# Kernel tuning notes

Hardware: AMD Instinct MI355X
Metric: run time of the kernel (lower is better)

## Reference

```python
import jax, jax.numpy as jnp
import numpy as np

N_NODES, N_EDGES = 100000, 800000
F_NODE, F_EDGE, N_CLASSES = 128, 16, 10


def _lin(key, fan_in, fan_out, bias=True):
    k1, k2 = jax.random.split(key)
    W = jax.random.normal(k1, (fan_in, fan_out), jnp.float32) * 0.05
    if bias:
        b = jax.random.normal(k2, (fan_out,), jnp.float32) * 0.05
        return W, b
    return (W,)


def setup_inputs() -> dict:
    key = jax.random.key(0)
    ks = jax.random.split(key, 24)
    inp = {
        "x": jax.random.normal(ks[0], (N_NODES, F_NODE), jnp.float32),
        "edge_index": jax.random.randint(ks[1], (2, N_EDGES), 0, N_NODES, jnp.int64 if jax.config.jax_enable_x64 else jnp.int32),
        "edge_attr": jax.random.normal(ks[2], (N_EDGES, F_EDGE), jnp.float32),
    }
    dims = [(F_NODE, 128), (128, 128), (128, 256)]  # (in_channels, out_channels) per layer
    i = 3
    for li, (din, dout) in enumerate(dims, start=1):
        inp[f"Wq{li}"], inp[f"bq{li}"] = _lin(ks[i], din, dout); i += 1
        inp[f"Wk{li}"], inp[f"bk{li}"] = _lin(ks[i], din, dout); i += 1
        inp[f"Wv{li}"], inp[f"bv{li}"] = _lin(ks[i], din, dout); i += 1
        (inp[f"We{li}"],) = _lin(ks[i], F_EDGE, dout, bias=False); i += 1  # PyG lin_edge: bias=False
        inp[f"Ws{li}"], inp[f"bs{li}"] = _lin(ks[i], din, dout); i += 1  # root/skip weight
    inp["Wc"], inp["bc"] = _lin(ks[i], 256, N_CLASSES)
    return inp


def transformer_conv(x, src, dst, edge_attr, Wq, bq, Wk, bk, Wv, bv, We, Ws, bs):
    """PyG TransformerConv, heads=1, concat=True, root_weight=True."""
    N = x.shape[0]
    C = Wq.shape[1]
    q = x @ Wq + bq                      # [N, C]
    k = x @ Wk + bk                      # [N, C]
    v = x @ Wv + bv                      # [N, C]
    e = edge_attr @ We                   # [E, C] edge-conditioned term
    # per-edge attention logits: <q_i, k_j + e_ij> / sqrt(C)
    alpha = jnp.sum(q[dst] * (k[src] + e), axis=-1) / jnp.sqrt(jnp.float32(C))  # [E]
    # segment softmax over edges sharing a destination node
    m = jax.ops.segment_max(alpha, dst, num_segments=N)
    p = jnp.exp(alpha - m[dst])
    s = jax.ops.segment_sum(p, dst, num_segments=N)
    a = p / (s[dst] + 1e-16)
    # scatter-aggregate weighted messages (value_j + edge term)
    out = jax.ops.segment_sum(a[:, None] * (v[src] + e), dst, num_segments=N)  # [N, C]
    return out + x @ Ws + bs             # root/skip connection


def reference(x, edge_index, edge_attr,
              Wq1, bq1, Wk1, bk1, Wv1, bv1, We1, Ws1, bs1,
              Wq2, bq2, Wk2, bk2, Wv2, bv2, We2, Ws2, bs2,
              Wq3, bq3, Wk3, bk3, Wv3, bv3, We3, Ws3, bs3,
              Wc, bc):
    src, dst = edge_index[0], edge_index[1]
    h = transformer_conv(x, src, dst, edge_attr, Wq1, bq1, Wk1, bk1, Wv1, bv1, We1, Ws1, bs1)
    h = jax.nn.relu(h)  # dropout is identity in eval mode
    h = transformer_conv(h, src, dst, edge_attr, Wq2, bq2, Wk2, bk2, Wv2, bv2, We2, Ws2, bs2)
    h = jax.nn.relu(h)
    h = transformer_conv(h, src, dst, edge_attr, Wq3, bq3, Wk3, bk3, Wv3, bv3, We3, Ws3, bs3)
    return h @ Wc + bc                   # [N, num_classes]
```

## Files before the change

kernel.cpp:

```cpp
#include <hip/hip_runtime.h>
#include <math.h>


typedef unsigned int uint;
typedef unsigned short ushort;
typedef __bf16 bf16x8 __attribute__((ext_vector_type(8)));
typedef float f32x4 __attribute__((ext_vector_type(4)));

__device__ __forceinline__ ushort f2bf(float f) {
    uint u = __float_as_uint(f);
    u += 0x7fffu + ((u >> 16) & 1u);
    return (ushort)(u >> 16);
}
__device__ __forceinline__ float bf2f(ushort h) {
    return __uint_as_float(((uint)h) << 16);
}
__device__ __forceinline__ void unpack8(uint4 t, float* o) {
    o[0] = bf2f((ushort)(t.x & 0xffffu)); o[1] = bf2f((ushort)(t.x >> 16));
    o[2] = bf2f((ushort)(t.y & 0xffffu)); o[3] = bf2f((ushort)(t.y >> 16));
    o[4] = bf2f((ushort)(t.z & 0xffffu)); o[5] = bf2f((ushort)(t.z >> 16));
    o[6] = bf2f((ushort)(t.w & 0xffffu)); o[7] = bf2f((ushort)(t.w >> 16));
}

__global__ void k_zero(uint* p, int n) {
    int i = blockIdx.x * 256 + threadIdx.x;
    if (i < n) p[i] = 0u;
}

__global__ void k_hist(const int* __restrict__ dst, uint* __restrict__ counts, int E, int N) {
    int e = blockIdx.x * 256 + threadIdx.x;
    if (e < E) {
        int d = dst[e];
        d = (d < 0) ? 0 : (d >= N ? N - 1 : d);
        atomicAdd(&counts[d], 1u);
    }
}

__global__ void k_scan1(const uint* __restrict__ counts, uint* __restrict__ bsum, int n) {
    __shared__ uint sm[256];
    int tid = threadIdx.x;
    int base = blockIdx.x * 1024 + tid * 4;
    uint s = 0;
#pragma unroll
    for (int j = 0; j < 4; ++j)
        if (base + j < n) s += counts[base + j];
    sm[tid] = s;
    __syncthreads();
    for (int d = 128; d > 0; d >>= 1) {
        if (tid < d) sm[tid] += sm[tid + d];
        __syncthreads();
    }
    if (tid == 0) bsum[blockIdx.x] = sm[0];
}

__global__ void k_scan2(uint* bsum, int nb) {
    if (threadIdx.x == 0 && blockIdx.x == 0) {
        uint run = 0;
        for (int i = 0; i < nb; ++i) { uint v = bsum[i]; bsum[i] = run; run += v; }
    }
}

__global__ void k_scan3(const uint* __restrict__ counts, const uint* __restrict__ bsum,
                        uint* __restrict__ row_ptr, int n, int E) {
    __shared__ uint sm[256];
    int tid = threadIdx.x;
    int base = blockIdx.x * 1024 + tid * 4;
    uint local[4];
    uint s = 0;
#pragma unroll
    for (int j = 0; j < 4; ++j) {
        local[j] = (base + j < n) ? counts[base + j] : 0u;
        s += local[j];
    }
    sm[tid] = s;
    __syncthreads();
    for (int d = 1; d < 256; d <<= 1) {
        uint v = (tid >= d) ? sm[tid - d] : 0u;
        __syncthreads();
        sm[tid] += v;
        __syncthreads();
    }
    uint run = sm[tid] - s + bsum[blockIdx.x];
#pragma unroll
    for (int j = 0; j < 4; ++j)
        if (base + j < n) { row_ptr[base + j] = run; run += local[j]; }
    if (blockIdx.x == 0 && tid == 0) row_ptr[n] = (uint)E;
}

__global__ void k_fill(const int* __restrict__ ei, const uint* __restrict__ row_ptr,
                       uint* __restrict__ cursor, int2* __restrict__ srcid, int E, int N) {
    int e = blockIdx.x * 256 + threadIdx.x;
    if (e >= E) return;
    int s = ei[e];
    int d = ei[E + e];
    s = (s < 0) ? 0 : (s >= N ? N - 1 : s);
    d = (d < 0) ? 0 : (d >= N ? N - 1 : d);
    uint idx = row_ptr[d] + atomicAdd(&cursor[d], 1u);
    srcid[idx] = make_int2(s, e);
}

__global__ void k_cvt(const float4* __restrict__ in, ushort4* __restrict__ outp, int n4) {
    int i = blockIdx.x * 256 + threadIdx.x;
    if (i >= n4) return;
    float4 v = in[i];
    ushort4 o;
    o.x = f2bf(v.x); o.y = f2bf(v.y); o.z = f2bf(v.z); o.w = f2bf(v.w);
    outp[i] = o;
}

__global__ void k_packg(const float* __restrict__ Wq, const float* __restrict__ bq,
                        const float* __restrict__ We, float* __restrict__ Wgf,
                        float* __restrict__ bgf, int C) {
    int id = blockIdx.x * 256 + threadIdx.x;
    if (id < 2048) {
        int k = id >> 4, f = id & 15;
        float s = 0.f;
        for (int c = 0; c < C; ++c) s = fmaf(Wq[k * C + c], We[f * C + c], s);
        Wgf[id] = s;
    } else if (id < 2064) {
        int f = id - 2048;
        float s = 0.f;
        for (int c = 0; c < C; ++c) s = fmaf(bq[c], We[f * C + c], s);
        bgf[f] = s;
    }
}

__global__ void k_packw(const float* __restrict__ Wq, const float* __restrict__ Wk,
                        const float* __restrict__ Wv, const float* __restrict__ Ws,
                        const float* __restrict__ Wgf, ushort* __restrict__ Bp, int C) {
    int nct = (4 * C + 16) >> 4;
    int total = 4 * nct * 512;
    int id = blockIdx.x * 256 + threadIdx.x;
    if (id >= total) return;
    int j = id & 7;
    int rest = id >> 3;
    int lane = rest & 63;
    rest >>= 6;
    int ct = rest % nct;
    int kt = rest / nct;
    int k = kt * 32 + ((lane >> 4) << 3) + j;
    int c = (ct << 4) + (lane & 15);
    float w;
    if (c < 4 * C) {
        int mat = c / C, cc = c % C;
        const float* W = (mat == 0) ? Wq : (mat == 1) ? Wk : (mat == 2) ? Wv : Ws;
        w = W[k * C + cc];
    } else {
        w = Wgf[k * 16 + (c - 4 * C)];
    }
    Bp[id] = f2bf(w);
}

__global__ void k_bias(const float* __restrict__ bq, const float* __restrict__ bk,
                       const float* __restrict__ bv, const float* __restrict__ bs,
                       const float* __restrict__ bgf, float* __restrict__ outp, int C) {
    int c = blockIdx.x * 256 + threadIdx.x;
    if (c >= 4 * C + 16) return;
    float v;
    if (c < 4 * C) {
        int mat = c / C, cc = c % C;
        const float* b = (mat == 0) ? bq : (mat == 1) ? bk : (mat == 2) ? bv : bs;
        v = b[cc];
    } else {
        v = bgf[c - 4 * C];
    }
    outp[c] = v;
}

__global__ __launch_bounds__(256) void k_gemm(const ushort* __restrict__ A,
                                              const ushort* __restrict__ Bp,
                                              const float* __restrict__ bias,
                                              ushort* __restrict__ H,
                                              ushort* __restrict__ S,
                                              ushort* __restrict__ g, int C) {
    int fourC = 4 * C, threeC = 3 * C;
    int P = fourC + 16;
    int nct = P >> 4;
    int lane = threadIdx.x & 63;
    int wave = threadIdx.x >> 6;
    int quad = lane >> 4;
    int r = lane & 15;
    int m0 = blockIdx.y << 4;
    int c0 = (blockIdx.x << 8) + (wave << 6);
    int ct0 = c0 >> 4;
    if (ct0 >= nct) return;
    int row = m0 + r;

    f32x4 acc[4];
#pragma unroll
    for (int i = 0; i < 4; ++i) acc[i] = (f32x4){0.f, 0.f, 0.f, 0.f};

#pragma unroll
    for (int kk = 0; kk < 4; ++kk) {
        bf16x8 a = *(const bf16x8*)(A + (size_t)row * 128 + kk * 32 + (quad << 3));
#pragma unroll
        for (int i = 0; i < 4; ++i) {
            if (ct0 + i < nct) {
                bf16x8 b = *(const bf16x8*)(Bp + ((size_t)((kk * nct + ct0 + i) << 6) + lane) * 8);
                acc[i] = __builtin_amdgcn_mfma_f32_16x16x32_bf16(a, b, acc[i], 0, 0, 0);
            }
        }
    }
#pragma unroll
    for (int i = 0; i < 4; ++i) {
        int cc = c0 + (i << 4) + r;
        if (cc >= P) continue;
        float bi = bias[cc];
#pragma unroll
        for (int reg = 0; reg < 4; ++reg) {
            int rr = m0 + (quad << 2) + reg;
            ushort val = f2bf(acc[i][reg] + bi);
            if (cc < threeC)      H[(size_t)rr * threeC + cc] = val;
            else if (cc < fourC)  S[(size_t)rr * C + (cc - threeC)] = val;
            else                  g[(size_t)rr * 16 + (cc - fourC)] = val;
        }
    }
}

template <int C, bool RELU>
__global__ __launch_bounds__(256) void k_edge(const ushort* __restrict__ H,
                                              ushort* __restrict__ S,
                                              const ushort* __restrict__ g,
                                              const uint* __restrict__ row_ptr,
                                              const int2* __restrict__ srcid,
                                              const float* __restrict__ eattr,
                                              const float* __restrict__ We,
                                              int N, int totalWaves) {
    constexpr int VR = C / 16;
    constexpr int NU4 = VR / 8;
    constexpr int TH = 3 * C;
    const float scale = (C == 128) ? 0.08838834764831843f : 0.0625f;
    int lane = threadIdx.x & 63;
    int sub = lane & 15;
    int quad = lane >> 4;
    int gw = (int)((blockIdx.x * blockDim.x + threadIdx.x) >> 6);

    for (int node = gw; node < N; node += totalWaves) {
        uint beg = row_ptr[node], end = row_ptr[node + 1];
        float q[VR];
        {
            const uint4* qp = (const uint4*)(H + (size_t)node * TH + sub * VR);
#pragma unroll
            for (int u = 0; u < NU4; ++u) { uint4 tt = qp[u]; unpack8(tt, q + u * 8); }
        }
        float gl = bf2f(g[(size_t)node * 16 + sub]);
        float m = -1e30f, l = 0.f, w = 0.f;
        float acc[VR];
#pragma unroll
        for (int j = 0; j < VR; ++j) acc[j] = 0.f;

        if (beg < end) {
            uint last = end - 1;
            uint i1 = beg + quad;     if (i1 > last) i1 = last;
            uint i2 = beg + 4 + quad; if (i2 > last) i2 = last;
            int2 seA = srcid[i1];
            int2 seB = srcid[i2];
            float atA = eattr[(size_t)seA.y * 16 + sub];
            uint4 kA[NU4], vA[NU4];
            {
                const uint4* kp = (const uint4*)(H + (size_t)seA.x * TH + C + sub * VR);
                const uint4* vp = (const uint4*)(H + (size_t)seA.x * TH + 2 * C + sub * VR);
#pragma unroll
                for (int u = 0; u < NU4; ++u) { kA[u] = kp[u]; vA[u] = vp[u]; }
            }
            for (uint t = beg; t < end; t += 4) {
                uint i3 = t + 8 + (uint)quad; if (i3 > last) i3 = last;
                int2 seC = srcid[i3];
                float atB = eattr[(size_t)seB.y * 16 + sub];
                uint4 kB[NU4], vB[NU4];
                {
                    const uint4* kp = (const uint4*)(H + (size_t)seB.x * TH + C + sub * VR);
                    const uint4* vp = (const uint4*)(H + (size_t)seB.x * TH + 2 * C + sub * VR);
#pragma unroll
                    for (int u = 0; u < NU4; ++u) { kB[u] = kp[u]; vB[u] = vp[u]; }
                }
                bool valid = (t + (uint)quad) < end;
                float kf[VR];
#pragma unroll
                for (int u = 0; u < NU4; ++u) unpack8(kA[u], kf + u * 8);
                float p = atA * gl;
#pragma unroll
                for (int j = 0; j < VR; ++j) p = fmaf(q[j], kf[j], p);
                p += __shfl_xor(p, 1);
                p += __shfl_xor(p, 2);
                p += __shfl_xor(p, 4);
                p += __shfl_xor(p, 8);
                float alpha = valid ? p * scale : -1e30f;
                float mn = fmaxf(m, alpha);
                float sc = __expf(m - mn);
                float e = valid ? __expf(alpha - mn) : 0.f;
                l = l * sc + e;
                w = fmaf(e, atA, w * sc);
                float vf[VR];
#pragma unroll
                for (int u = 0; u < NU4; ++u) unpack8(vA[u], vf + u * 8);
#pragma unroll
                for (int j = 0; j < VR; ++j) acc[j] = fmaf(e, vf[j], acc[j] * sc);
                m = mn;
                seB = seC;
                atA = atB;
#pragma unroll
                for (int u = 0; u < NU4; ++u) { kA[u] = kB[u]; vA[u] = vB[u]; }
            }
            float mm = fmaxf(m, __shfl_xor(m, 16));
            mm = fmaxf(mm, __shfl_xor(mm, 32));
            float r = __expf(m - mm);
            l *= r; l += __shfl_xor(l, 16); l += __shfl_xor(l, 32);
            w *= r; w += __shfl_xor(w, 16); w += __shfl_xor(w, 32);
#pragma unroll
            for (int j = 0; j < VR; ++j) {
                float a = acc[j] * r;
                a += __shfl_xor(a, 16);
                a += __shfl_xor(a, 32);
                acc[j] = a;
            }
        }
        float inv = 1.f / (l + 1e-16f);
        float ew[VR];
#pragma unroll
        for (int j = 0; j < VR; ++j) ew[j] = 0.f;
#pragma unroll
        for (int i = 0; i < 4; ++i) {
            int f = quad * 4 + i;
            float wf = __shfl(w, f);
            const float* wrow = We + f * C + sub * VR;
#pragma unroll
            for (int u = 0; u < VR / 4; ++u) {
                float4 cv = *(const float4*)(wrow + u * 4);
                ew[u * 4 + 0] = fmaf(wf, cv.x, ew[u * 4 + 0]);
                ew[u * 4 + 1] = fmaf(wf, cv.y, ew[u * 4 + 1]);
                ew[u * 4 + 2] = fmaf(wf, cv.z, ew[u * 4 + 2]);
                ew[u * 4 + 3] = fmaf(wf, cv.w, ew[u * 4 + 3]);
            }
        }
#pragma unroll
        for (int j = 0; j < VR; ++j) {
            ew[j] += __shfl_xor(ew[j], 16);
            ew[j] += __shfl_xor(ew[j], 32);
        }
        if (quad == 0) {
            ushort* srow = S + (size_t)node * C + sub * VR;
#pragma unroll
            for (int u = 0; u < NU4; ++u) {
                uint4 skv = *(const uint4*)(srow + u * 8);
                float sk[8];
                unpack8(skv, sk);
                uint4 ov;
                uint* op = (uint*)&ov;
#pragma unroll
                for (int h = 0; h < 4; ++h) {
                    float o0 = (acc[u * 8 + 2 * h] + ew[u * 8 + 2 * h]) * inv + sk[2 * h];
                    float o1 = (acc[u * 8 + 2 * h + 1] + ew[u * 8 + 2 * h + 1]) * inv + sk[2 * h + 1];
                    if (RELU) { o0 = fmaxf(o0, 0.f); o1 = fmaxf(o1, 0.f); }
                    op[h] = (uint)f2bf(o0) | ((uint)f2bf(o1) << 16);
                }
                *(uint4*)(srow + u * 8) = ov;
            }
        }
    }
}

__global__ void k_cls(const ushort* __restrict__ h, const float* __restrict__ Wc,
                      const float* __restrict__ bc, float* __restrict__ outp, int N) {
    int t = blockIdx.x * 256 + threadIdx.x;
    int node = t >> 4;
    int c = t & 15;
    if (node >= N || c >= 10) return;
    const ushort* hr = h + (size_t)node * 256;
    float acc = 0.f;
#pragma unroll 4
    for (int k4 = 0; k4 < 64; ++k4) {
        uint2 u = *(const uint2*)(hr + k4 * 4);
        float h0 = bf2f((ushort)(u.x & 0xffffu));
        float h1 = bf2f((ushort)(u.x >> 16));
        float h2 = bf2f((ushort)(u.y & 0xffffu));
        float h3 = bf2f((ushort)(u.y >> 16));
        int kb = k4 * 4;
        acc = fmaf(h0, Wc[(kb + 0) * 10 + c], acc);
        acc = fmaf(h1, Wc[(kb + 1) * 10 + c], acc);
        acc = fmaf(h2, Wc[(kb + 2) * 10 + c], acc);
        acc = fmaf(h3, Wc[(kb + 3) * 10 + c], acc);
    }
    outp[node * 10 + c] = acc + bc[c];
}

extern "C" void kernel_launch(void* const* d_in, const int* in_sizes, int n_in,
                              void* d_out, int out_size, void* d_ws, size_t ws_size,
                              hipStream_t stream) {
    const float* x = (const float*)d_in[0];
    const int* ei = (const int*)d_in[1];
    const float* eattr = (const float*)d_in[2];
    const int N = in_sizes[0] / 128;
    const int E = in_sizes[1] / 2;

    const float* Wq[3], *bq[3], *Wk[3], *bk[3], *Wv[3], *bv[3], *We[3], *Ws[3], *bs[3];
    for (int li = 0; li < 3; ++li) {
        int base = 3 + li * 9;
        Wq[li] = (const float*)d_in[base + 0];
        bq[li] = (const float*)d_in[base + 1];
        Wk[li] = (const float*)d_in[base + 2];
        bk[li] = (const float*)d_in[base + 3];
        Wv[li] = (const float*)d_in[base + 4];
        bv[li] = (const float*)d_in[base + 5];
        We[li] = (const float*)d_in[base + 6];
        Ws[li] = (const float*)d_in[base + 7];
        bs[li] = (const float*)d_in[base + 8];
    }
    const float* Wc = (const float*)d_in[30];
    const float* bc = (const float*)d_in[31];

    size_t off = 0;
    char* base = (char*)d_ws;
    auto alloc = [&](size_t bytes) -> void* {
        void* p = base + off;
        off = (off + bytes + 255) & ~(size_t)255;
        return p;
    };
    ushort* SA = (ushort*)alloc((size_t)N * 256 * 2);
    ushort* SB = (ushort*)alloc((size_t)N * 128 * 2);
    ushort* H  = (ushort*)alloc((size_t)N * 768 * 2);
    ushort* gbuf = (ushort*)alloc((size_t)N * 16 * 2);
    ushort* Bp = (ushort*)alloc(140000 * 2);
    float* biasc = (float*)alloc(1040 * 4);
    float* Wgf = (float*)alloc(2048 * 4);
    float* bgf = (float*)alloc(16 * 4);
    uint* row_ptr = (uint*)alloc((size_t)(N + 1) * 4);
    uint* counts = (uint*)alloc((size_t)N * 4);
    uint* cursor = (uint*)alloc((size_t)N * 4);
    uint* bsum = (uint*)alloc(1024 * 4);
    int2* srcid = (int2*)alloc((size_t)E * 8);

    ushort* xb = SB;

    int nb = (N + 1023) / 1024;

    k_zero<<<(N + 255) / 256, 256, 0, stream>>>(counts, N);
    k_zero<<<(N + 255) / 256, 256, 0, stream>>>(cursor, N);
    k_hist<<<(E + 255) / 256, 256, 0, stream>>>(ei + E, counts, E, N);
    k_scan1<<<nb, 256, 0, stream>>>(counts, bsum, N);
    k_scan2<<<1, 64, 0, stream>>>(bsum, nb);
    k_scan3<<<nb, 256, 0, stream>>>(counts, bsum, row_ptr, N, E);
    k_fill<<<(E + 255) / 256, 256, 0, stream>>>(ei, row_ptr, cursor, srcid, E, N);

    int n4 = N * 128 / 4;
    k_cvt<<<(n4 + 255) / 256, 256, 0, stream>>>((const float4*)x, (ushort4*)xb, n4);

    const int EDGE_BLOCKS = 2048;
    const int TW = EDGE_BLOCKS * 4;

    for (int li = 0; li < 3; ++li) {
        int C = (li == 2) ? 256 : 128;
        int P = 4 * C + 16;
        int packTotal = 4 * (P >> 4) * 512;
        const ushort* A = (li == 0) ? xb : (li == 1) ? SA : SB;
        ushort* Sout = (li == 1) ? SB : SA;

        k_packg<<<9, 256, 0, stream>>>(Wq[li], bq[li], We[li], Wgf, bgf, C);
        k_packw<<<(packTotal + 255) / 256, 256, 0, stream>>>(Wq[li], Wk[li], Wv[li], Ws[li], Wgf, Bp, C);
        k_bias<<<(P + 255) / 256, 256, 0, stream>>>(bq[li], bk[li], bv[li], bs[li], bgf, biasc, C);
        k_gemm<<<dim3((P + 255) / 256, N / 16), 256, 0, stream>>>(A, Bp, biasc, H, Sout, gbuf, C);
        if (li == 2)
            k_edge<256, false><<<EDGE_BLOCKS, 256, 0, stream>>>(H, Sout, gbuf, row_ptr, srcid, eattr, We[li], N, TW);
        else
            k_edge<128, true><<<EDGE_BLOCKS, 256, 0, stream>>>(H, Sout, gbuf, row_ptr, srcid, eattr, We[li], N, TW);
    }

    k_cls<<<(N * 16 + 255) / 256, 256, 0, stream>>>(SA, Wc, bc, (float*)d_out, N);
}
```

Measured before the change: 1.126 ms.

## Assign one 16-lane group per node in edge kernel with 3-deep prefetch

```diff
diff --git a/kernel.cpp b/kernel.cpp
--- a/kernel.cpp
+++ b/kernel.cpp
@@ -225,17 +225,17 @@
                                               const int2* __restrict__ srcid,
                                               const float* __restrict__ eattr,
                                               const float* __restrict__ We,
-                                              int N, int totalWaves) {
+                                              int N, int totalGroups) {
     constexpr int VR = C / 16;
     constexpr int NU4 = VR / 8;
     constexpr int TH = 3 * C;
     const float scale = (C == 128) ? 0.08838834764831843f : 0.0625f;
     int lane = threadIdx.x & 63;
     int sub = lane & 15;
-    int quad = lane >> 4;
-    int gw = (int)((blockIdx.x * blockDim.x + threadIdx.x) >> 6);
-
-    for (int node = gw; node < N; node += totalWaves) {
+    int gbase = lane & 48;
+    int gg = (int)((blockIdx.x * 256 + threadIdx.x) >> 4);
+
+    for (int node = gg; node < N; node += totalGroups) {
         uint beg = row_ptr[node], end = row_ptr[node + 1];
         float q[VR];
         {
@@ -251,68 +251,63 @@
 
         if (beg < end) {
             uint last = end - 1;
-            uint i1 = beg + quad;     if (i1 > last) i1 = last;
-            uint i2 = beg + 4 + quad; if (i2 > last) i2 = last;
-            int2 seA = srcid[i1];
-            int2 seB = srcid[i2];
-            float atA = eattr[(size_t)seA.y * 16 + sub];
-            uint4 kA[NU4], vA[NU4];
+            int2 se0 = srcid[beg];
+            int2 se1 = srcid[(beg + 1 > last) ? last : beg + 1];
+            int2 se2 = srcid[(beg + 2 > last) ? last : beg + 2];
+            float at0 = eattr[(size_t)se0.y * 16 + sub];
+            float at1 = eattr[(size_t)se1.y * 16 + sub];
+            uint4 k0[NU4], v0[NU4], k1[NU4], v1[NU4];
             {
-                const uint4* kp = (const uint4*)(H + (size_t)seA.x * TH + C + sub * VR);
-                const uint4* vp = (const uint4*)(H + (size_t)seA.x * TH + 2 * C + sub * VR);
-#pragma unroll
-                for (int u = 0; u < NU4; ++u) { kA[u] = kp[u]; vA[u] = vp[u]; }
-            }
-            for (uint t = beg; t < end; t += 4) {
-                uint i3 = t + 8 + (uint)quad; if (i3 > last) i3 = last;
-                int2 seC = srcid[i3];
-                float atB = eattr[(size_t)seB.y * 16 + sub];
-                uint4 kB[NU4], vB[NU4];
-                {
-                    const uint4* kp = (const uint4*)(H + (size_t)seB.x * TH + C + sub * VR);
-                    const uint4* vp = (const uint4*)(H + (size_t)seB.x * TH + 2 * C + sub * VR);
-#pragma unroll
-                    for (int u = 0; u < NU4; ++u) { kB[u] = kp[u]; vB[u] = vp[u]; }
+                const uint4* kp = (const uint4*)(H + (size_t)se0.x * TH + C + sub * VR);
+                const uint4* vp = (const uint4*)(H + (size_t)se0.x * TH + 2 * C + sub * VR);
+#pragma unroll
+                for (int u = 0; u < NU4; ++u) { k0[u] = kp[u]; v0[u] = vp[u]; }
+            }
+            if (beg + 1 <= last) {
+                const uint4* kp = (const uint4*)(H + (size_t)se1.x * TH + C + sub * VR);
+                const uint4* vp = (const uint4*)(H + (size_t)se1.x * TH + 2 * C + sub * VR);
+#pragma unroll
+                for (int u = 0; u < NU4; ++u) { k1[u] = kp[u]; v1[u] = vp[u]; }
+            }
+            for (uint t = beg; t < end; ++t) {
+                uint t3 = (t + 3 > last) ? last : t + 3;
+                int2 se3 = srcid[t3];
+                float at2 = eattr[(size_t)se2.y * 16 + sub];
+                uint4 k2[NU4], v2[NU4];
+                if (t + 2 <= last) {
+                    const uint4* kp = (const uint4*)(H + (size_t)se2.x * TH + C + sub * VR);
+                    const uint4* vp = (const uint4*)(H + (size_t)se2.x * TH + 2 * C + sub * VR);
+#pragma unroll
+                    for (int u = 0; u < NU4; ++u) { k2[u] = kp[u]; v2[u] = vp[u]; }
                 }
-                bool valid = (t + (uint)quad) < end;
                 float kf[VR];
 #pragma unroll
-                for (int u = 0; u < NU4; ++u) unpack8(kA[u], kf + u * 8);
-                float p = atA * gl;
+                for (int u = 0; u < NU4; ++u) unpack8(k0[u], kf + u * 8);
+                float p = at0 * gl;
 #pragma unroll
                 for (int j = 0; j < VR; ++j) p = fmaf(q[j], kf[j], p);
                 p += __shfl_xor(p, 1);
                 p += __shfl_xor(p, 2);
                 p += __shfl_xor(p, 4);
                 p += __shfl_xor(p, 8);
-                float alpha = valid ? p * scale : -1e30f;
+                float alpha = p * scale;
                 float mn = fmaxf(m, alpha);
                 float sc = __expf(m - mn);
-                float e = valid ? __expf(alpha - mn) : 0.f;
+                float e = __expf(alpha - mn);
                 l = l * sc + e;
-                w = fmaf(e, atA, w * sc);
+                w = fmaf(e, at0, w * sc);
                 float vf[VR];
 #pragma unroll
-                for (int u = 0; u < NU4; ++u) unpack8(vA[u], vf + u * 8);
+                for (int u = 0; u < NU4; ++u) unpack8(v0[u], vf + u * 8);
 #pragma unroll
                 for (int j = 0; j < VR; ++j) acc[j] = fmaf(e, vf[j], acc[j] * sc);
                 m = mn;
-                seB = seC;
-                atA = atB;
-#pragma unroll
-                for (int u = 0; u < NU4; ++u) { kA[u] = kB[u]; vA[u] = vB[u]; }
-            }
-            float mm = fmaxf(m, __shfl_xor(m, 16));
-            mm = fmaxf(mm, __shfl_xor(mm, 32));
-            float r = __expf(m - mm);
-            l *= r; l += __shfl_xor(l, 16); l += __shfl_xor(l, 32);
-            w *= r; w += __shfl_xor(w, 16); w += __shfl_xor(w, 32);
-#pragma unroll
-            for (int j = 0; j < VR; ++j) {
-                float a = acc[j] * r;
-                a += __shfl_xor(a, 16);
-                a += __shfl_xor(a, 32);
-                acc[j] = a;
+#pragma unroll
+                for (int u = 0; u < NU4; ++u) {
+                    k0[u] = k1[u]; v0[u] = v1[u];
+                    k1[u] = k2[u]; v1[u] = v2[u];
+                }
+                at0 = at1; at1 = at2; se2 = se3;
             }
         }
         float inv = 1.f / (l + 1e-16f);
@@ -320,9 +315,8 @@
 #pragma unroll
         for (int j = 0; j < VR; ++j) ew[j] = 0.f;
 #pragma unroll
-        for (int i = 0; i < 4; ++i) {
-            int f = quad * 4 + i;
-            float wf = __shfl(w, f);
+        for (int f = 0; f < 16; ++f) {
+            float wf = __shfl(w, gbase | f);
             const float* wrow = We + f * C + sub * VR;
 #pragma unroll
             for (int u = 0; u < VR / 4; ++u) {
@@ -333,29 +327,22 @@
                 ew[u * 4 + 3] = fmaf(wf, cv.w, ew[u * 4 + 3]);
             }
         }
-#pragma unroll
-        for (int j = 0; j < VR; ++j) {
-            ew[j] += __shfl_xor(ew[j], 16);
-            ew[j] += __shfl_xor(ew[j], 32);
-        }
-        if (quad == 0) {
-            ushort* srow = S + (size_t)node * C + sub * VR;
-#pragma unroll
-            for (int u = 0; u < NU4; ++u) {
-                uint4 skv = *(const uint4*)(srow + u * 8);
-                float sk[8];
-                unpack8(skv, sk);
-                uint4 ov;
-                uint* op = (uint*)&ov;
-#pragma unroll
-                for (int h = 0; h < 4; ++h) {
-                    float o0 = (acc[u * 8 + 2 * h] + ew[u * 8 + 2 * h]) * inv + sk[2 * h];
-                    float o1 = (acc[u * 8 + 2 * h + 1] + ew[u * 8 + 2 * h + 1]) * inv + sk[2 * h + 1];
-                    if (RELU) { o0 = fmaxf(o0, 0.f); o1 = fmaxf(o1, 0.f); }
-                    op[h] = (uint)f2bf(o0) | ((uint)f2bf(o1) << 16);
-                }
-                *(uint4*)(srow + u * 8) = ov;
-            }
+        ushort* srow = S + (size_t)node * C + sub * VR;
+#pragma unroll
+        for (int u = 0; u < NU4; ++u) {
+            uint4 skv = *(const uint4*)(srow + u * 8);
+            float sk[8];
+            unpack8(skv, sk);
+            uint4 ov;
+            uint* op = (uint*)&ov;
+#pragma unroll
+            for (int h = 0; h < 4; ++h) {
+                float o0 = (acc[u * 8 + 2 * h] + ew[u * 8 + 2 * h]) * inv + sk[2 * h];
+                float o1 = (acc[u * 8 + 2 * h + 1] + ew[u * 8 + 2 * h + 1]) * inv + sk[2 * h + 1];
+                if (RELU) { o0 = fmaxf(o0, 0.f); o1 = fmaxf(o1, 0.f); }
+                op[h] = (uint)f2bf(o0) | ((uint)f2bf(o1) << 16);
+            }
+            *(uint4*)(srow + u * 8) = ov;
         }
     }
 }
@@ -445,8 +432,8 @@
     int n4 = N * 128 / 4;
     k_cvt<<<(n4 + 255) / 256, 256, 0, stream>>>((const float4*)x, (ushort4*)xb, n4);
 
-    const int EDGE_BLOCKS = 2048;
-    const int TW = EDGE_BLOCKS * 4;
+    const int EDGE_BLOCKS = 4096;
+    const int TG = EDGE_BLOCKS * 16;
 
     for (int li = 0; li < 3; ++li) {
         int C = (li == 2) ? 256 : 128;
@@ -460,9 +447,9 @@
         k_bias<<<(P + 255) / 256, 256, 0, stream>>>(bq[li], bk[li], bv[li], bs[li], bgf, biasc, C);
         k_gemm<<<dim3((P + 255) / 256, N / 16), 256, 0, stream>>>(A, Bp, biasc, H, Sout, gbuf, C);
         if (li == 2)
-            k_edge<256, false><<<EDGE_BLOCKS, 256, 0, stream>>>(H, Sout, gbuf, row_ptr, srcid, eattr, We[li], N, TW);
+            k_edge<256, false><<<EDGE_BLOCKS, 256, 0, stream>>>(H, Sout, gbuf, row_ptr, srcid, eattr, We[li], N, TG);
         else
-            k_edge<128, true><<<EDGE_BLOCKS, 256, 0, stream>>>(H, Sout, gbuf, row_ptr, srcid, eattr, We[li], N, TW);
+            k_edge<128, true><<<EDGE_BLOCKS, 256, 0, stream>>>(H, Sout, gbuf, row_ptr, srcid, eattr, We[li], N, TG);
     }
 
     k_cls<<<(N * 16 + 255) / 256, 256, 0, stream>>>(SA, Wc, bc, (float*)d_out, N);
```

New measurement: 1.260 ms. +11.9%, slower.
